# Kernel tuning notes

Measured on AMD Instinct MI355X. Metric: run time of the kernel, lower is better.

## Reference

```python
import jax, jax.numpy as jnp
import numpy as np

B, S, D, H, HD = 4, 2048, 1024, 16, 64
MLP = 4 * D
ROPE_BASE = 10000.0
TARGET_SPARSITY = 0.2


def _rotate_half(t):
    return jnp.concatenate([-t[..., HD // 2:], t[..., :HD // 2]], axis=-1)


def setup_inputs() -> dict:
    key = jax.random.key(0)
    ks = jax.random.split(key, 10)
    s = 0.02
    return {
        "x": jax.random.normal(ks[0], (B, S, D), jnp.float32),
        "gate_w": jax.random.normal(ks[1], (D, 1), jnp.float32) * s,
        "gate_b": jnp.zeros((1,), jnp.float32),
        "wq": jax.random.normal(ks[2], (D, D), jnp.float32) * s,
        "wk": jax.random.normal(ks[3], (D, D), jnp.float32) * s,
        "wv": jax.random.normal(ks[4], (D, D), jnp.float32) * s,
        "wo": jax.random.normal(ks[5], (D, D), jnp.float32) * s,
        "conv_w": jax.random.normal(ks[6], (D, 3), jnp.float32) * s,  # depthwise k=3
        "conv_b": jnp.zeros((D,), jnp.float32),
        "mlp_w1": jax.random.normal(ks[7], (D, MLP), jnp.float32) * s,
        "mlp_b1": jnp.zeros((MLP,), jnp.float32),
        "mlp_w2": jax.random.normal(ks[8], (MLP, D), jnp.float32) * s,
        "mlp_b2": jnp.zeros((D,), jnp.float32),
    }


def reference(x, gate_w, gate_b, wq, wk, wv, wo, conv_w, conv_b,
              mlp_w1, mlp_b1, mlp_w2, mlp_b2):
    # --- Router (eval path: hard threshold, mask_ste == active mask) ---
    logits = x @ gate_w + gate_b                    # [B,S,1]
    probs = jax.nn.sigmoid(logits)
    aux_loss = (probs.mean() - TARGET_SPARSITY) ** 2
    mask = (probs > 0.5).astype(x.dtype)            # [B,S,1]

    # --- Reflexive stream: causal depthwise conv (left pad 2) + MLP ---
    xp = jnp.pad(x, ((0, 0), (2, 0), (0, 0)))       # [B,S+2,D]
    x_conv = (xp[:, 0:S] * conv_w[:, 0]
              + xp[:, 1:S + 1] * conv_w[:, 1]
              + xp[:, 2:S + 2] * conv_w[:, 2] + conv_b)
    shallow = jax.nn.relu(x_conv @ mlp_w1 + mlp_b1) @ mlp_w2 + mlp_b2

    # --- Contextual stream: RoPE causal attention, queries gated by router ---
    q = (x @ wq).reshape(B, S, H, HD)
    k = (x @ wk).reshape(B, S, H, HD)
    v = (x @ wv).reshape(B, S, H, HD)

    pos = jnp.arange(S)
    inv_freq = 1.0 / (ROPE_BASE ** (jnp.arange(0, HD, 2, dtype=jnp.float32) / HD))
    freqs = pos[:, None].astype(jnp.float32) * inv_freq[None, :]
    emb = jnp.concatenate([freqs, freqs], axis=-1)  # [S,HD]
    cos = jnp.cos(emb)[None, :, None, :]
    sin = jnp.sin(emb)[None, :, None, :]
    q = q * cos + _rotate_half(q) * sin
    k = k * cos + _rotate_half(k) * sin

    scale = 1.0 / np.sqrt(HD)
    scores = jnp.einsum('bqhd,bkhd->bhqk', q, k) * scale
    causal = pos[:, None] >= pos[None, :]           # [S,S]
    scores = jnp.where(causal[None, None], scores, jnp.finfo(scores.dtype).min)
    attn = jax.nn.softmax(scores, axis=-1)
    ctx = jnp.einsum('bhqk,bkhd->bqhd', attn, v).reshape(B, S, D)
    ctx = (ctx @ wo) * mask                         # scatter back: only active queries contribute

    out = x + shallow + ctx
    return out, aux_loss
```

## Files before the change

### kernel.cpp

```cpp
#include <hip/hip_runtime.h>
#include <hip/hip_bf16.h>

#define DDIM 1024
#define SLEN 2048
#define NTOK 8192
#define MLPD 4096

typedef float f32x4 __attribute__((ext_vector_type(4)));
typedef __bf16 bf16x8 __attribute__((ext_vector_type(8)));

__device__ __forceinline__ void async16(void* lds, const void* g) {
  __builtin_amdgcn_global_load_lds(
      (__attribute__((address_space(1))) void*)g,
      (__attribute__((address_space(3))) void*)lds, 16, 0, 0);
}

template <int N> struct VMC { static constexpr int v = N; };

__global__ __launch_bounds__(256) void prep_kernel(
    const float* __restrict__ x, const float* __restrict__ gate_w,
    const float* __restrict__ gate_b, const float* __restrict__ conv_w,
    const float* __restrict__ conv_b, __bf16* __restrict__ xb,
    __bf16* __restrict__ xcb, float* __restrict__ maskp,
    float* __restrict__ probsp) {
  const int tok = blockIdx.x, t = threadIdx.x;
  const int s = tok & (SLEN - 1);
  const float* xr = x + (size_t)tok * DDIM;
  float4 v = ((const float4*)xr)[t];
  float4 g = ((const float4*)gate_w)[t];
  float part = v.x * g.x + v.y * g.y + v.z * g.z + v.w * g.w;
#pragma unroll
  for (int d = 32; d; d >>= 1) part += __shfl_down(part, d);
  __shared__ float ws4[4];
  const int lane = t & 63, w = t >> 6;
  if (lane == 0) ws4[w] = part;
  __syncthreads();
  if (t == 0) {
    float logit = ws4[0] + ws4[1] + ws4[2] + ws4[3] + gate_b[0];
    float prob = 1.f / (1.f + __expf(-logit));
    probsp[tok] = prob;
    maskp[tok] = prob > 0.5f ? 1.f : 0.f;
  }
  union { ushort4 u; __bf16 b[4]; } xo;
  xo.b[0] = (__bf16)v.x; xo.b[1] = (__bf16)v.y;
  xo.b[2] = (__bf16)v.z; xo.b[3] = (__bf16)v.w;
  ((ushort4*)(xb + (size_t)tok * DDIM))[t] = xo.u;
  float4 zero4 = {0.f, 0.f, 0.f, 0.f};
  float4 m1 = (s >= 1) ? ((const float4*)(xr - DDIM))[t] : zero4;
  float4 m2 = (s >= 2) ? ((const float4*)(xr - 2 * DDIM))[t] : zero4;
  int d0 = t * 4;
  float vv[4] = {v.x, v.y, v.z, v.w};
  float a1[4] = {m1.x, m1.y, m1.z, m1.w};
  float a2[4] = {m2.x, m2.y, m2.z, m2.w};
  union { ushort4 u; __bf16 b[4]; } co;
#pragma unroll
  for (int i = 0; i < 4; ++i) {
    float c0 = conv_w[(d0 + i) * 3 + 0];
    float c1 = conv_w[(d0 + i) * 3 + 1];
    float c2 = conv_w[(d0 + i) * 3 + 2];
    float r = a2[i] * c0 + a1[i] * c1 + vv[i] * c2 + conv_b[d0 + i];
    co.b[i] = (__bf16)r;
  }
  ((ushort4*)(xcb + (size_t)tok * DDIM))[t] = co.u;
}

__global__ __launch_bounds__(256) void tcast_kernel(const float* __restrict__ src,
                                                    __bf16* __restrict__ dst,
                                                    int K, int N) {
  __shared__ __bf16 tile[64][65];
  const int n0 = blockIdx.x * 64, k0 = blockIdx.y * 64;
  const int t = threadIdx.x;
  const int cr = (t & 15) * 4;
#pragma unroll
  for (int i = 0; i < 4; ++i) {
    int rr = (t >> 4) + i * 16;
    float4 v = *(const float4*)(src + (size_t)(k0 + rr) * N + n0 + cr);
    tile[rr][cr + 0] = (__bf16)v.x; tile[rr][cr + 1] = (__bf16)v.y;
    tile[rr][cr + 2] = (__bf16)v.z; tile[rr][cr + 3] = (__bf16)v.w;
  }
  __syncthreads();
#pragma unroll
  for (int i = 0; i < 2; ++i) {
    int c = t + i * 256;
    int nl = c >> 3, koff = (c & 7) * 8;
    union { uint4 u; __bf16 b[8]; } o;
#pragma unroll
    for (int j = 0; j < 8; ++j) o.b[j] = tile[koff + j][nl];
    *(uint4*)(dst + (size_t)(n0 + nl) * K + k0 + koff) = o.u;
  }
}

template <int EPI>
__global__ __launch_bounds__(512, 2) void gemm256p(
    const __bf16* __restrict__ A, const __bf16* __restrict__ Bt,
    const float* __restrict__ bias, __bf16* __restrict__ Cb,
    int M, int N, int K) {
  extern __shared__ char sm[];
  const int t = threadIdx.x, lane = t & 63, w = t >> 6;
  const int c = lane & 15, g = lane >> 4;
  const int nwg = gridDim.x * gridDim.y;
  const int wgid = blockIdx.y * gridDim.x + blockIdx.x;
  const int swz = (wgid & 7) * (nwg >> 3) + (wgid >> 3);
  const int m0 = (swz / gridDim.x) * 256, n0 = (swz % gridDim.x) * 256;
  const int wm = (w >> 2) * 128, wn = (w & 3) * 64;

  f32x4 acc[8][4] = {};
  const int nk = K >> 5;

  auto stage = [&](int buf, int kt) {
    const int k0 = kt << 5;
    char* base = sm + buf * 32768;
#pragma unroll
    for (int r = 0; r < 2; ++r) {
      int o = ((r * 8 + w) << 10) + (lane << 4);
      int rp = o >> 7;
      int u = (o >> 4) & 7;
      int l = u ^ (rp & 7);
      int mr = rp * 2 + (l >> 2);
      int kk = (l & 3) * 8;
      async16(base + o, A + (size_t)(m0 + mr) * K + k0 + kk);
      async16(base + 16384 + o, Bt + (size_t)(n0 + mr) * K + k0 + kk);
    }
  };

  auto body = [&](auto vmc, int tt, bool dostage) {
    if (dostage) stage((tt + 3) & 3, tt + 3);
    asm volatile("s_waitcnt vmcnt(%0)" ::"n"(decltype(vmc)::v) : "memory");
    __builtin_amdgcn_s_barrier();
    asm volatile("" ::: "memory");
    const char* Ab = sm + (tt & 3) * 32768;
    const char* Bb = Ab + 16384;
    bf16x8 aq[8], bq[4];
#pragma unroll
    for (int nt = 0; nt < 4; ++nt) {
      int row = wn + nt * 16 + c;
      int rp = row >> 1;
      int u = ((row & 1) * 4 + g) ^ (rp & 7);
      bq[nt] = *(const bf16x8*)(Bb + rp * 128 + u * 16);
    }
#pragma unroll
    for (int i = 0; i < 8; ++i) {
      int row = wm + i * 16 + c;
      int rp = row >> 1;
      int u = ((row & 1) * 4 + g) ^ (rp & 7);
      aq[i] = *(const bf16x8*)(Ab + rp * 128 + u * 16);
    }
    __builtin_amdgcn_s_setprio(1);
#pragma unroll
    for (int i = 0; i < 8; ++i)
#pragma unroll
      for (int nt = 0; nt < 4; ++nt)
        acc[i][nt] = __builtin_amdgcn_mfma_f32_16x16x32_bf16(
            aq[i], bq[nt], acc[i][nt], 0, 0, 0);
    __builtin_amdgcn_s_setprio(0);
    __builtin_amdgcn_s_barrier();
    asm volatile("" ::: "memory");
  };

  stage(0, 0);
  stage(1, 1);
  stage(2, 2);
  int tt = 0;
  for (; tt < nk - 3; ++tt) body(VMC<12>{}, tt, true);
  body(VMC<8>{}, tt, false); ++tt;
  body(VMC<4>{}, tt, false); ++tt;
  body(VMC<0>{}, tt, false);

#pragma unroll
  for (int i = 0; i < 8; ++i)
#pragma unroll
    for (int nt = 0; nt < 4; ++nt)
#pragma unroll
      for (int r = 0; r < 4; ++r) {
        int row = m0 + wm + i * 16 + g * 4 + r;
        int col = n0 + wn + nt * 16 + c;
        float v = acc[i][nt][r];
        size_t idx = (size_t)row * N + col;
        if constexpr (EPI == 0) {
          Cb[idx] = (__bf16)v;
        } else {
          v += bias[col];
          Cb[idx] = (__bf16)fmaxf(v, 0.f);
        }
      }
}

template <int EPI>
__global__ __launch_bounds__(256, 3) void gemm_bt(
    const __bf16* __restrict__ A, const __bf16* __restrict__ Bt,
    const float* __restrict__ bias, const float* __restrict__ xres,
    const float* __restrict__ maskp, __bf16* __restrict__ Cb,
    float* __restrict__ Cf, int M, int N, int K) {
  __shared__ char smem[32768];
  char* As = smem;
  char* Bs = smem + 16384;
  const int t = threadIdx.x, lane = t & 63, w = t >> 6;
  const int nwg = gridDim.x * gridDim.y;
  const int wgid = blockIdx.y * gridDim.x + blockIdx.x;
  const int swz = (wgid & 7) * (nwg >> 3) + (wgid >> 3);
  const int m0 = (swz / gridDim.x) * 128, n0 = (swz % gridDim.x) * 128;
  const int wm = (w >> 1) * 64, wn = (w & 1) * 64;
  f32x4 acc[4][4] = {};
  const int nk = K >> 6;
  for (int kt = 0; kt < nk; ++kt) {
    const int k0 = kt << 6;
#pragma unroll
    for (int rd = 0; rd < 4; ++rd) {
      int o = ((rd * 4 + w) << 10) + (lane << 4);
      int row = o >> 7;
      int us = ((o >> 4) & 7) ^ (row & 7);
      async16(As + o, A + (size_t)(m0 + row) * K + k0 + us * 8);
      async16(Bs + o, Bt + (size_t)(n0 + row) * K + k0 + us * 8);
    }
    __syncthreads();
#pragma unroll
    for (int ks = 0; ks < 2; ++ks) {
      bf16x8 af[4], bfr[4];
#pragma unroll
      for (int mt = 0; mt < 4; ++mt) {
        int row = wm + mt * 16 + (lane & 15);
        int u = (ks * 4 + (lane >> 4)) ^ (row & 7);
        af[mt] = *(const bf16x8*)(As + row * 128 + u * 16);
      }
#pragma unroll
      for (int nt = 0; nt < 4; ++nt) {
        int row = wn + nt * 16 + (lane & 15);
        int u = (ks * 4 + (lane >> 4)) ^ (row & 7);
        bfr[nt] = *(const bf16x8*)(Bs + row * 128 + u * 16);
      }
#pragma unroll
      for (int mt = 0; mt < 4; ++mt)
#pragma unroll
        for (int nt = 0; nt < 4; ++nt)
          acc[mt][nt] = __builtin_amdgcn_mfma_f32_16x16x32_bf16(
              af[mt], bfr[nt], acc[mt][nt], 0, 0, 0);
    }
    __syncthreads();
  }
#pragma unroll
  for (int mt = 0; mt < 4; ++mt)
#pragma unroll
    for (int nt = 0; nt < 4; ++nt)
#pragma unroll
      for (int r = 0; r < 4; ++r) {
        int row = m0 + wm + mt * 16 + ((lane >> 4) << 2) + r;
        int col = n0 + wn + nt * 16 + (lane & 15);
        float v = acc[mt][nt][r];
        size_t idx = (size_t)row * N + col;
        if constexpr (EPI == 2) {
          Cf[idx] = xres[idx] + v + bias[col];
        } else {
          Cf[idx] += maskp[row] * v;
        }
      }
}

__global__ __launch_bounds__(256) void rope_kernel(__bf16* __restrict__ qkv) {
  __shared__ float snv[32], csv[32];
  const int tok = blockIdx.x, t = threadIdx.x;
  const int s = tok & (SLEN - 1);
  if (t < 32) {
    float invf = __builtin_amdgcn_exp2f(-(float)t * (13.28771238f / 32.f));
    float fr = (float)s * invf;
    snv[t] = sinf(fr);
    csv[t] = cosf(fr);
  }
  __syncthreads();
#pragma unroll
  for (int pp = 0; pp < 2; ++pp) {
    int p = t + pp * 256;
    int h = p >> 5, i = p & 31;
    float sn = snv[i], cs = csv[i];
    __bf16* qp = qkv + (size_t)tok * 3072 + h * 64 + i;
    float xq = (float)qp[0], yq = (float)qp[32];
    qp[0] = (__bf16)(xq * cs - yq * sn);
    qp[32] = (__bf16)(yq * cs + xq * sn);
    __bf16* kp = qp + 1024;
    float xk = (float)kp[0], yk = (float)kp[32];
    kp[0] = (__bf16)(xk * cs - yk * sn);
    kp[32] = (__bf16)(yk * cs + xk * sn);
  }
}

__device__ __forceinline__ void scatterV(char* Vdst, int w, int lane,
                                         float4 va, float4 vb) {
  union { float4 f; __bf16 bv[8]; } u0, u1;
  u0.f = va; u1.f = vb;
#pragma unroll
  for (int j = 0; j < 8; ++j) {
    int d = w * 8 + j;
    int by = d * 128 + (((lane >> 3) ^ (d & 7)) << 4) + ((lane & 7) << 1);
    *(__bf16*)(Vdst + by) = u0.bv[j];
    int d2 = d + 32;
    int by2 = d2 * 128 + (((lane >> 3) ^ (d2 & 7)) << 4) + ((lane & 7) << 1);
    *(__bf16*)(Vdst + by2) = u1.bv[j];
  }
}

__global__ __launch_bounds__(256, 3) void attn_kernel(const __bf16* __restrict__ qkv,
                                                      __bf16* __restrict__ ctx) {
  __shared__ char sm[32768];
  const int t = threadIdx.x, lane = t & 63, w = t >> 6;
  const int c = lane & 15, g = lane >> 4, g4 = g * 4;
  const int bh = blockIdx.y, h = bh & 15, b = bh >> 4;
  const size_t tokbase = (size_t)b * SLEN;
  const __bf16* qg = qkv + tokbase * 3072 + h * 64;
  const __bf16* kg = qg + 1024;
  const __bf16* vg = qg + 2048;
  const float SCL = 0.125f * 1.44269504f;
  char* Ps = sm + (w << 12);
  char* Ks = sm + 16384;
  char* Vs = sm + 24576;

  for (int ph = 0; ph < 2; ++ph) {
    const int qt = ph == 0 ? (int)blockIdx.x : 15 - (int)blockIdx.x;
    const int q0 = qt * 128;
#pragma unroll
    for (int rd = 0; rd < 4; ++rd) {
      int o = ((rd * 4 + w) << 10) + (lane << 4);
      int row = o >> 7;
      int us = ((o >> 4) & 7) ^ (row & 7);
      async16(sm + o, qg + (size_t)(q0 + row) * 3072 + us * 8);
    }
    __syncthreads();
    bf16x8 qb[2][2];
#pragma unroll
    for (int mt = 0; mt < 2; ++mt)
#pragma unroll
      for (int ks = 0; ks < 2; ++ks) {
        int row = w * 32 + mt * 16 + c;
        int u = (ks * 4 + g) ^ (row & 7);
        qb[mt][ks] = *(const bf16x8*)(sm + row * 128 + u * 16);
      }

    float m_run[2] = {-1e30f, -1e30f}, l_run[2] = {0.f, 0.f};
    f32x4 o_acc[2][4] = {};
    const int nkt = (q0 + 128) >> 6;
    const int wrow0 = q0 + w * 32;

    for (int kt = 0; kt < nkt; ++kt) {
      const int k0 = kt << 6;
#pragma unroll
      for (int rd = 0; rd < 2; ++rd) {
        int o = ((rd * 4 + w) << 10) + (lane << 4);
        int row = o >> 7;
        int us = ((o >> 4) & 7) ^ (row & 7);
        async16(Ks + o, kg + (size_t)(k0 + row) * 3072 + us * 8);
      }
      {
        float4 va = *(const float4*)(vg + (size_t)(k0 + lane) * 3072 + w * 8);
        float4 vb2 = *(const float4*)(vg + (size_t)(k0 + lane) * 3072 + w * 8 + 32);
        scatterV(Vs, w, lane, va, vb2);
      }
      __syncthreads();
      if (k0 <= wrow0 + 31) {
        f32x4 st[4][2] = {};
        __builtin_amdgcn_s_setprio(1);
#pragma unroll
        for (int ks = 0; ks < 2; ++ks) {
          bf16x8 ka[4];
#pragma unroll
          for (int nt = 0; nt < 4; ++nt) {
            int row = nt * 16 + c;
            int u = (ks * 4 + g) ^ (row & 7);
            ka[nt] = *(const bf16x8*)(Ks + row * 128 + u * 16);
          }
#pragma unroll
          for (int nt = 0; nt < 4; ++nt)
#pragma unroll
            for (int mt = 0; mt < 2; ++mt)
              st[nt][mt] = __builtin_amdgcn_mfma_f32_16x16x32_bf16(
                  ka[nt], qb[mt][ks], st[nt][mt], 0, 0, 0);
        }
        __builtin_amdgcn_s_setprio(0);
        const bool needmask = (k0 + 63) > wrow0;
#pragma unroll
        for (int mt = 0; mt < 2; ++mt) {
          float mx = -1e30f;
          if (needmask) {
            int qglob = wrow0 + mt * 16 + c;
#pragma unroll
            for (int nt = 0; nt < 4; ++nt)
#pragma unroll
              for (int r = 0; r < 4; ++r) {
                float sv = st[nt][mt][r] * SCL;
                if (k0 + nt * 16 + g4 + r > qglob) sv = -1e30f;
                st[nt][mt][r] = sv;
                mx = fmaxf(mx, sv);
              }
          } else {
#pragma unroll
            for (int nt = 0; nt < 4; ++nt)
#pragma unroll
              for (int r = 0; r < 4; ++r) {
                float sv = st[nt][mt][r] * SCL;
                st[nt][mt][r] = sv;
                mx = fmaxf(mx, sv);
              }
          }
          mx = fmaxf(mx, __shfl_xor(mx, 16));
          mx = fmaxf(mx, __shfl_xor(mx, 32));
          const bool skip = __all(mx - m_run[mt] <= 8.f) != 0;
          float mnew = skip ? m_run[mt] : fmaxf(m_run[mt], mx);
          float rs = 0.f;
#pragma unroll
          for (int nt = 0; nt < 4; ++nt)
#pragma unroll
            for (int r = 0; r < 4; ++r) {
              float p = __builtin_amdgcn_exp2f(st[nt][mt][r] - mnew);
              st[nt][mt][r] = p;
              rs += p;
            }
          rs += __shfl_xor(rs, 16);
          rs += __shfl_xor(rs, 32);
          if (skip) {
            l_run[mt] += rs;
          } else {
            float fac = __builtin_amdgcn_exp2f(m_run[mt] - mnew);
            m_run[mt] = mnew;
            l_run[mt] = l_run[mt] * fac + rs;
#pragma unroll
            for (int r = 0; r < 4; ++r) {
              float fr = __shfl(fac, g * 20 + r);
#pragma unroll
              for (int dt = 0; dt < 4; ++dt) o_acc[mt][dt][r] *= fr;
            }
          }
          int rowq = mt * 16 + c;
          int rbase = rowq * 128 + 8 * (g & 1);
#pragma unroll
          for (int nt = 0; nt < 4; ++nt) {
            int us = (2 * nt + (g >> 1)) ^ (c & 7);
            union { uint2 v; __bf16 bb[4]; } pp;
            pp.bb[0] = (__bf16)st[nt][mt][0]; pp.bb[1] = (__bf16)st[nt][mt][1];
            pp.bb[2] = (__bf16)st[nt][mt][2]; pp.bb[3] = (__bf16)st[nt][mt][3];
            *(uint2*)(Ps + rbase + us * 16) = pp.v;
          }
        }
        __builtin_amdgcn_s_setprio(1);
#pragma unroll
        for (int ks = 0; ks < 2; ++ks) {
          bf16x8 pa[2], vb[4];
#pragma unroll
          for (int mt = 0; mt < 2; ++mt) {
            int row = mt * 16 + c;
            int u = (ks * 4 + g) ^ (row & 7);
            pa[mt] = *(const bf16x8*)(Ps + row * 128 + u * 16);
          }
#pragma unroll
          for (int dt = 0; dt < 4; ++dt) {
            int row = dt * 16 + c;
            int u = (ks * 4 + g) ^ (row & 7);
            vb[dt] = *(const bf16x8*)(Vs + row * 128 + u * 16);
          }
#pragma unroll
          for (int mt = 0; mt < 2; ++mt)
#pragma unroll
            for (int dt = 0; dt < 4; ++dt)
              o_acc[mt][dt] = __builtin_amdgcn_mfma_f32_16x16x32_bf16(
                  pa[mt], vb[dt], o_acc[mt][dt], 0, 0, 0);
        }
        __builtin_amdgcn_s_setprio(0);
      }
      __syncthreads();
    }
#pragma unroll
    for (int mt = 0; mt < 2; ++mt)
#pragma unroll
      for (int r = 0; r < 4; ++r) {
        float lr = __shfl(l_run[mt], g * 20 + r);
        float inv = 1.f / lr;
        int tokr = q0 + w * 32 + mt * 16 + g4 + r;
#pragma unroll
        for (int dt = 0; dt < 4; ++dt) {
          int d = dt * 16 + c;
          ctx[(tokbase + tokr) * DDIM + h * 64 + d] =
              (__bf16)(o_acc[mt][dt][r] * inv);
        }
      }
  }
}

__global__ __launch_bounds__(256) void aux_kernel(const float* __restrict__ probsp,
                                                  float* __restrict__ outp) {
  const int t = threadIdx.x;
  float sum = 0.f;
  for (int i = t; i < NTOK; i += 256) sum += probsp[i];
#pragma unroll
  for (int d = 32; d; d >>= 1) sum += __shfl_down(sum, d);
  __shared__ float ws4[4];
  if ((t & 63) == 0) ws4[t >> 6] = sum;
  __syncthreads();
  if (t == 0) {
    float m = (ws4[0] + ws4[1] + ws4[2] + ws4[3]) * (1.f / NTOK) - 0.2f;
    outp[0] = m * m;
  }
}

extern "C" void kernel_launch(void* const* d_in, const int* in_sizes, int n_in,
                              void* d_out, int out_size, void* d_ws, size_t ws_size,
                              hipStream_t stream) {
  const float* x      = (const float*)d_in[0];
  const float* gate_w = (const float*)d_in[1];
  const float* gate_b = (const float*)d_in[2];
  const float* wq     = (const float*)d_in[3];
  const float* wk     = (const float*)d_in[4];
  const float* wv     = (const float*)d_in[5];
  const float* wo     = (const float*)d_in[6];
  const float* conv_w = (const float*)d_in[7];
  const float* conv_b = (const float*)d_in[8];
  const float* mlp_w1 = (const float*)d_in[9];
  const float* mlp_b1 = (const float*)d_in[10];
  const float* mlp_w2 = (const float*)d_in[11];
  const float* mlp_b2 = (const float*)d_in[12];
  float* out = (float*)d_out;

  char* ws = (char*)d_ws;
  const size_t MB = 1ull << 20;
  __bf16* xb     = (__bf16*)(ws + 0);
  __bf16* xcb    = (__bf16*)(ws + 16 * MB);
  __bf16* ctx    = (__bf16*)(ws + 16 * MB);
  __bf16* wqkv_t = (__bf16*)(ws + 32 * MB);
  __bf16* wo_t   = (__bf16*)(ws + 38 * MB);
  __bf16* w1_t   = (__bf16*)(ws + 40 * MB);
  __bf16* w2_t   = (__bf16*)(ws + 48 * MB);
  float*  maskp  = (float*)(ws + 56 * MB);
  float*  probsp = (float*)(ws + 56 * MB + 65536);
  __bf16* h1     = (__bf16*)(ws + 57 * MB);
  __bf16* qkv    = (__bf16*)(ws + 57 * MB);

  prep_kernel<<<NTOK, 256, 0, stream>>>(x, gate_w, gate_b, conv_w, conv_b,
                                        xb, xcb, maskp, probsp);
  tcast_kernel<<<dim3(16, 16), 256, 0, stream>>>(wq, wqkv_t, 1024, 1024);
  tcast_kernel<<<dim3(16, 16), 256, 0, stream>>>(wk, wqkv_t + 1024 * 1024, 1024, 1024);
  tcast_kernel<<<dim3(16, 16), 256, 0, stream>>>(wv, wqkv_t + 2048 * 1024, 1024, 1024);
  tcast_kernel<<<dim3(16, 16), 256, 0, stream>>>(wo, wo_t, 1024, 1024);
  tcast_kernel<<<dim3(64, 16), 256, 0, stream>>>(mlp_w1, w1_t, 1024, 4096);
  tcast_kernel<<<dim3(16, 64), 256, 0, stream>>>(mlp_w2, w2_t, 4096, 1024);

  gemm256p<1><<<dim3(16, 32), 512, 131072, stream>>>(xcb, w1_t, mlp_b1, h1,
                                                     NTOK, MLPD, DDIM);
  gemm_bt<2><<<dim3(8, 64), 256, 0, stream>>>(h1, w2_t, mlp_b2, x, nullptr,
                                              nullptr, out, NTOK, DDIM, MLPD);
  gemm256p<0><<<dim3(12, 32), 512, 131072, stream>>>(xb, wqkv_t, nullptr, qkv,
                                                     NTOK, 3072, DDIM);
  rope_kernel<<<NTOK, 256, 0, stream>>>(qkv);
  attn_kernel<<<dim3(8, 64), 256, 0, stream>>>(qkv, ctx);
  gemm_bt<3><<<dim3(8, 64), 256, 0, stream>>>(ctx, wo_t, nullptr, nullptr, maskp,
                                              nullptr, out, NTOK, DDIM, DDIM);
  aux_kernel<<<1, 256, 0, stream>>>(probsp, out + (size_t)(out_size - 1));
}
```

Before: 405.7 us.

## Fuse RoPE into QKV GEMM epilogue using precomputed cos/sin table

Removes the standalone rope kernel, which re-read and re-wrote the Q and K halves of the qkv buffer. RoPE is now applied in registers in the QKV GEMM epilogue, using a small cos/sin table generated once per call by a new kernel. The rotation is done before the bf16 rounding, which slightly changes numerics. The attention grid index mapping is also remapped so consecutive blocks cover different batch-heads for the same query-tile pair, which may change L2 locality.

After: 393.4 us, median of 2. 3.0% less time.

```diff
diff --git a/kernel.cpp b/kernel.cpp
--- a/kernel.cpp
+++ b/kernel.cpp
@@ -64,6 +64,14 @@
   ((ushort4*)(xcb + (size_t)tok * DDIM))[t] = co.u;
 }
 
+__global__ __launch_bounds__(256) void tabgen_kernel(float2* __restrict__ tab) {
+  const int idx = blockIdx.x * 256 + threadIdx.x;
+  const int s = idx >> 5, i = idx & 31;
+  float invf = __builtin_amdgcn_exp2f(-(float)i * (13.28771238f / 32.f));
+  float fr = (float)s * invf;
+  tab[idx] = make_float2(cosf(fr), sinf(fr));
+}
+
 __global__ __launch_bounds__(256) void tcast_kernel(const float* __restrict__ src,
                                                     __bf16* __restrict__ dst,
                                                     int K, int N) {
@@ -90,11 +98,11 @@
   }
 }
 
-template <int EPI>
+template <int EPI, bool ROPE>
 __global__ __launch_bounds__(512, 2) void gemm256p(
     const __bf16* __restrict__ A, const __bf16* __restrict__ Bt,
-    const float* __restrict__ bias, __bf16* __restrict__ Cb,
-    int M, int N, int K) {
+    const float* __restrict__ bias, const float2* __restrict__ tab,
+    __bf16* __restrict__ Cb, int M, int N, int K) {
   extern __shared__ char sm[];
   const int t = threadIdx.x, lane = t & 63, w = t >> 6;
   const int c = lane & 15, g = lane >> 4;
@@ -165,6 +173,23 @@
   body(VMC<8>{}, tt, false); ++tt;
   body(VMC<4>{}, tt, false); ++tt;
   body(VMC<0>{}, tt, false);
+
+  if (ROPE && n0 < 2048) {
+#pragma unroll
+    for (int i = 0; i < 8; ++i)
+#pragma unroll
+      for (int r = 0; r < 4; ++r) {
+        int s = (m0 + wm + i * 16 + g * 4 + r) & (SLEN - 1);
+        float2 t0 = tab[s * 32 + c];
+        float2 t1 = tab[s * 32 + 16 + c];
+        float q0 = acc[i][0][r], q2 = acc[i][2][r];
+        acc[i][0][r] = q0 * t0.x - q2 * t0.y;
+        acc[i][2][r] = q2 * t0.x + q0 * t0.y;
+        float q1 = acc[i][1][r], q3 = acc[i][3][r];
+        acc[i][1][r] = q1 * t1.x - q3 * t1.y;
+        acc[i][3][r] = q3 * t1.x + q1 * t1.y;
+      }
+  }
 
 #pragma unroll
   for (int i = 0; i < 8; ++i)
@@ -255,33 +280,6 @@
       }
 }
 
-__global__ __launch_bounds__(256) void rope_kernel(__bf16* __restrict__ qkv) {
-  __shared__ float snv[32], csv[32];
-  const int tok = blockIdx.x, t = threadIdx.x;
-  const int s = tok & (SLEN - 1);
-  if (t < 32) {
-    float invf = __builtin_amdgcn_exp2f(-(float)t * (13.28771238f / 32.f));
-    float fr = (float)s * invf;
-    snv[t] = sinf(fr);
-    csv[t] = cosf(fr);
-  }
-  __syncthreads();
-#pragma unroll
-  for (int pp = 0; pp < 2; ++pp) {
-    int p = t + pp * 256;
-    int h = p >> 5, i = p & 31;
-    float sn = snv[i], cs = csv[i];
-    __bf16* qp = qkv + (size_t)tok * 3072 + h * 64 + i;
-    float xq = (float)qp[0], yq = (float)qp[32];
-    qp[0] = (__bf16)(xq * cs - yq * sn);
-    qp[32] = (__bf16)(yq * cs + xq * sn);
-    __bf16* kp = qp + 1024;
-    float xk = (float)kp[0], yk = (float)kp[32];
-    kp[0] = (__bf16)(xk * cs - yk * sn);
-    kp[32] = (__bf16)(yk * cs + xk * sn);
-  }
-}
-
 __device__ __forceinline__ void scatterV(char* Vdst, int w, int lane,
                                          float4 va, float4 vb) {
   union { float4 f; __bf16 bv[8]; } u0, u1;
@@ -302,7 +300,9 @@
   __shared__ char sm[32768];
   const int t = threadIdx.x, lane = t & 63, w = t >> 6;
   const int c = lane & 15, g = lane >> 4, g4 = g * 4;
-  const int bh = blockIdx.y, h = bh & 15, b = bh >> 4;
+  const int bh = (int)blockIdx.x * 8 + ((int)blockIdx.y & 7);
+  const int qp = (int)blockIdx.y >> 3;
+  const int h = bh & 15, b = bh >> 4;
   const size_t tokbase = (size_t)b * SLEN;
   const __bf16* qg = qkv + tokbase * 3072 + h * 64;
   const __bf16* kg = qg + 1024;
@@ -313,7 +313,7 @@
   char* Vs = sm + 24576;
 
   for (int ph = 0; ph < 2; ++ph) {
-    const int qt = ph == 0 ? (int)blockIdx.x : 15 - (int)blockIdx.x;
+    const int qt = ph == 0 ? qp : 15 - qp;
     const int q0 = qt * 128;
 #pragma unroll
     for (int rd = 0; rd < 4; ++rd) {
@@ -526,11 +526,13 @@
   __bf16* w2_t   = (__bf16*)(ws + 48 * MB);
   float*  maskp  = (float*)(ws + 56 * MB);
   float*  probsp = (float*)(ws + 56 * MB + 65536);
+  float2* ropetab= (float2*)(ws + 56 * MB + 131072);
   __bf16* h1     = (__bf16*)(ws + 57 * MB);
   __bf16* qkv    = (__bf16*)(ws + 57 * MB);
 
   prep_kernel<<<NTOK, 256, 0, stream>>>(x, gate_w, gate_b, conv_w, conv_b,
                                         xb, xcb, maskp, probsp);
+  tabgen_kernel<<<256, 256, 0, stream>>>(ropetab);
   tcast_kernel<<<dim3(16, 16), 256, 0, stream>>>(wq, wqkv_t, 1024, 1024);
   tcast_kernel<<<dim3(16, 16), 256, 0, stream>>>(wk, wqkv_t + 1024 * 1024, 1024, 1024);
   tcast_kernel<<<dim3(16, 16), 256, 0, stream>>>(wv, wqkv_t + 2048 * 1024, 1024, 1024);
@@ -538,13 +540,12 @@
   tcast_kernel<<<dim3(64, 16), 256, 0, stream>>>(mlp_w1, w1_t, 1024, 4096);
   tcast_kernel<<<dim3(16, 64), 256, 0, stream>>>(mlp_w2, w2_t, 4096, 1024);
 
-  gemm256p<1><<<dim3(16, 32), 512, 131072, stream>>>(xcb, w1_t, mlp_b1, h1,
-                                                     NTOK, MLPD, DDIM);
+  gemm256p<1, false><<<dim3(16, 32), 512, 131072, stream>>>(
+      xcb, w1_t, mlp_b1, nullptr, h1, NTOK, MLPD, DDIM);
   gemm_bt<2><<<dim3(8, 64), 256, 0, stream>>>(h1, w2_t, mlp_b2, x, nullptr,
                                               nullptr, out, NTOK, DDIM, MLPD);
-  gemm256p<0><<<dim3(12, 32), 512, 131072, stream>>>(xb, wqkv_t, nullptr, qkv,
-                                                     NTOK, 3072, DDIM);
-  rope_kernel<<<NTOK, 256, 0, stream>>>(qkv);
+  gemm256p<0, true><<<dim3(12, 32), 512, 131072, stream>>>(
+      xb, wqkv_t, nullptr, ropetab, qkv, NTOK, 3072, DDIM);
   attn_kernel<<<dim3(8, 64), 256, 0, stream>>>(qkv, ctx);
   gemm_bt<3><<<dim3(8, 64), 256, 0, stream>>>(ctx, wo_t, nullptr, nullptr, maskp,
                                               nullptr, out, NTOK, DDIM, DDIM);
```
